# Performance work log

Hardware: AMD Instinct MI355X
Metric: run time of the kernel (lower is better)

The kernel has to match this reference:

```python
import jax, jax.numpy as jnp
import numpy as np

H = 1024      # hidden_size
NH = 16       # num_heads
HD = H // NH  # head_dim


def setup_inputs() -> dict:
    key = jax.random.key(0)
    ks = jax.random.split(key, 12)
    inp = {
        "query": jax.random.normal(ks[0], (4, 1024, H), dtype=jnp.float32),
        "key": jax.random.normal(ks[1], (4, 2048, H), dtype=jnp.float32),
        "value": jax.random.normal(ks[2], (4, 2048, H), dtype=jnp.float32),
        "key_padding_mask": jax.random.randint(ks[3], (4, 2048), 0, 2, dtype=jnp.int32),
        # learned parameters (torch Linear: y = x @ W.T + b); we store W already transposed
        "Wq": jax.random.normal(ks[4], (H, H), dtype=jnp.float32) * (1.0 / np.sqrt(H)),
        "bq": jnp.zeros((H,), dtype=jnp.float32),
        "Wk": jax.random.normal(ks[5], (H, H), dtype=jnp.float32) * (1.0 / np.sqrt(H)),
        "bk": jnp.zeros((H,), dtype=jnp.float32),
        "Wv": jax.random.normal(ks[6], (H, H), dtype=jnp.float32) * (1.0 / np.sqrt(H)),
        "bv": jnp.zeros((H,), dtype=jnp.float32),
        "Wo": jax.random.normal(ks[7], (H, H), dtype=jnp.float32) * (1.0 / np.sqrt(H)),
        "bo": jnp.zeros((H,), dtype=jnp.float32),
    }
    return inp


def reference(query, key, value, key_padding_mask, Wq, bq, Wk, bk, Wv, bv, Wo, bo):
    B, Sq, _ = query.shape
    Sk = key.shape[1]
    scaling = HD ** -0.5
    # projections -> [B, NH, S, HD]
    q = (query @ Wq + bq).reshape(B, Sq, NH, HD).transpose(0, 2, 1, 3)
    k = (key @ Wk + bk).reshape(B, Sk, NH, HD).transpose(0, 2, 1, 3)
    v = (value @ Wv + bv).reshape(B, Sk, NH, HD).transpose(0, 2, 1, 3)
    # scores [B, NH, Sq, Sk]
    scores = jnp.einsum("bhqd,bhkd->bhqk", q, k) * scaling
    # mask: positions where key_padding_mask == 0 are ignored
    scores = jnp.where((key_padding_mask == 0)[:, None, None, :], -jnp.inf, scores)
    attn = jax.nn.softmax(scores, axis=-1)
    # dropout is identity in eval mode
    out = jnp.einsum("bhqk,bhkd->bhqd", attn, v)
    out = out.transpose(0, 2, 1, 3).reshape(B, Sq, H)
    return out @ Wo + bo
```

## Files before the change

kernel.cpp:

```cpp
#include <hip/hip_runtime.h>
#include <hip/hip_fp16.h>
#include <math.h>

#define B_ 4
#define SQ 1024
#define SK 2048
#define HH 1024
#define NHEAD 16
#define HDIM 64

typedef _Float16 f16;
typedef __attribute__((ext_vector_type(8))) _Float16 f16x8;
typedef __attribute__((ext_vector_type(4))) _Float16 f16x4;
typedef __attribute__((ext_vector_type(4))) float f32x4;
typedef unsigned int u32;

#define GLOAD_LDS16(gp, lp) __builtin_amdgcn_global_load_lds( \
    (const __attribute__((address_space(1))) u32*)(gp),        \
    (__attribute__((address_space(3))) u32*)(lp), 16, 0, 0)
#define GLOAD_LDS4(gp, lp) __builtin_amdgcn_global_load_lds(  \
    (const __attribute__((address_space(1))) u32*)(gp),        \
    (__attribute__((address_space(3))) u32*)(lp), 4, 0, 0)

__global__ __launch_bounds__(256) void prep_k(
    const float* __restrict__ q, const float* __restrict__ k,
    const float* __restrict__ v,
    const float* __restrict__ W0, const float* __restrict__ W1,
    const float* __restrict__ W2, const float* __restrict__ W3,
    const int* __restrict__ mask,
    f16* __restrict__ qo, f16* __restrict__ ko, f16* __restrict__ vo,
    f16* __restrict__ WT, float* __restrict__ pbias)
{
    __shared__ f16 t[64 * 80];
    const int bid = blockIdx.x, tid = threadIdx.x;
    if (bid < 10240) {
        int i = bid * 256 + tid;
        const float* src; f16* dst; int j;
        if (i < 524288)       { src = q; dst = qo; j = i; }
        else if (i < 1572864) { src = k; dst = ko; j = i - 524288; }
        else                  { src = v; dst = vo; j = i - 1572864; }
        float4 a = ((const float4*)src)[(size_t)j * 2];
        float4 b = ((const float4*)src)[(size_t)j * 2 + 1];
        f16x8 o;
        o[0] = (f16)a.x; o[1] = (f16)a.y; o[2] = (f16)a.z; o[3] = (f16)a.w;
        o[4] = (f16)b.x; o[5] = (f16)b.y; o[6] = (f16)b.z; o[7] = (f16)b.w;
        *(f16x8*)(dst + (size_t)j * 8) = o;
    } else if (bid < 11264) {
        int id = bid - 10240;
        int z = id >> 8, idx = id & 255;
        const float* W = z == 0 ? W0 : z == 1 ? W1 : z == 2 ? W2 : W3;
        f16* out = WT + (size_t)z * HH * HH;
        const int r0 = (idx >> 4) * 64, c0 = (idx & 15) * 64;
#pragma unroll
        for (int p = 0; p < 4; p++) {
            int s = p * 256 + tid;
            int row = s >> 4, u = s & 15;
            float4 a = *(const float4*)(W + (size_t)(r0 + row) * HH + c0 + u * 4);
            f16x4 vv;
            vv[0] = (f16)a.x; vv[1] = (f16)a.y; vv[2] = (f16)a.z; vv[3] = (f16)a.w;
            *(f16x4*)(t + row * 80 + u * 4) = vv;
        }
        __syncthreads();
#pragma unroll
        for (int p = 0; p < 2; p++) {
            int s = p * 256 + tid;
            int n = s >> 3, u = s & 7;
            f16x8 vv;
#pragma unroll
            for (int j = 0; j < 8; j++) vv[j] = t[(u * 8 + j) * 80 + n];
            *(f16x8*)(out + (size_t)(c0 + n) * HH + r0 + u * 8) = vv;
        }
    } else {
        int j = (bid - 11264) * 256 + tid;
        pbias[j] = mask[j] ? 0.f : -1e30f;
    }
}

template <int TM, int OUTMODE>
__device__ __forceinline__ void gemm_body(
    const f16* __restrict__ A, const f16* __restrict__ BT,
    const float* __restrict__ bias, void* __restrict__ Cout,
    int bid, int nwg, f16* sA, f16* sB)
{
    const int tid = threadIdx.x, lane = tid & 63, w = tid >> 6;
    const int swz = (bid & 7) * (nwg >> 3) + (bid >> 3);
    const int m0 = (swz >> 3) * TM;
    const int n0 = (swz & 7) * 128;
    const int wr = w >> 1, wc = w & 1;
    const int ql = lane & 15, g = lane >> 4;
    const int N = 1024, K = 1024;
    const int MF = TM / 32;
    const int ABUF = TM * 32;
    f32x4 acc[MF][4] = {};

    auto stageA = [&](int buf, int k0) {
#pragma unroll
        for (int p = 0; p < TM / 64; p++) {
            int s = p * 256 + tid;
            int row = s >> 2, us = ((s & 3) ^ ((row >> 1) & 3)) * 8;
            GLOAD_LDS16(A + (size_t)(m0 + row) * K + k0 + us,
                        sA + buf * ABUF + (p * 256 + w * 64) * 8);
        }
    };
    auto stageB = [&](int buf, int k0) {
#pragma unroll
        for (int p = 0; p < 2; p++) {
            int s = p * 256 + tid;
            int row = s >> 2, us = ((s & 3) ^ ((row >> 1) & 3)) * 8;
            GLOAD_LDS16(BT + (size_t)(n0 + row) * K + k0 + us,
                        sB + buf * 4096 + (p * 256 + w * 64) * 8);
        }
    };
    auto compute = [&](int buf) {
        f16x8 af[MF], bf[4];
#pragma unroll
        for (int m = 0; m < MF; m++) {
            int row = wr * (TM / 2) + m * 16 + ql;
            af[m] = *(const f16x8*)(sA + buf * ABUF + row * 32 + ((g ^ ((row >> 1) & 3)) * 8));
        }
#pragma unroll
        for (int n = 0; n < 4; n++) {
            int row = wc * 64 + n * 16 + ql;
            bf[n] = *(const f16x8*)(sB + buf * 4096 + row * 32 + ((g ^ ((row >> 1) & 3)) * 8));
        }
#pragma unroll
        for (int m = 0; m < MF; m++)
#pragma unroll
            for (int n = 0; n < 4; n++)
                acc[m][n] = __builtin_amdgcn_mfma_f32_16x16x32_f16(af[m], bf[n], acc[m][n], 0, 0, 0);
    };

    stageA(0, 0);
    stageB(0, 0);
    int cur = 0;
#pragma unroll 1
    for (int k0 = 0; k0 < K; k0 += 32) {
        __syncthreads();
        if (k0 + 32 < K) { stageA(cur ^ 1, k0 + 32); stageB(cur ^ 1, k0 + 32); }
        compute(cur);
        cur ^= 1;
    }

    float bv[4];
#pragma unroll
    for (int n = 0; n < 4; n++) bv[n] = bias[n0 + wc * 64 + n * 16 + ql];
#pragma unroll
    for (int m = 0; m < MF; m++) {
        int row0 = m0 + wr * (TM / 2) + m * 16 + g * 4;
#pragma unroll
        for (int n = 0; n < 4; n++) {
            int col = n0 + wc * 64 + n * 16 + ql;
            if (OUTMODE == 2) {
                int bb = row0 >> 11, kk = row0 & 2047;
                int hh = col >> 6, dd = col & 63;
                f16x4 vv;
#pragma unroll
                for (int e = 0; e < 4; e++) vv[e] = (f16)(acc[m][n][e] + bv[n]);
                *(f16x4*)((f16*)Cout + ((size_t)(bb * NHEAD + hh) * HDIM + dd) * SK + kk) = vv;
            } else if (OUTMODE == 1) {
#pragma unroll
                for (int e = 0; e < 4; e++)
                    ((f16*)Cout)[(size_t)(row0 + e) * N + col] = (f16)(acc[m][n][e] + bv[n]);
            } else {
#pragma unroll
                for (int e = 0; e < 4; e++)
                    ((float*)Cout)[(size_t)(row0 + e) * N + col] = acc[m][n][e] + bv[n];
            }
        }
    }
}

__global__ __launch_bounds__(256) void qkv_gemm_k(
    const f16* __restrict__ qc, const f16* __restrict__ kc,
    const f16* __restrict__ vc, const f16* __restrict__ wT,
    const float* __restrict__ bq, const float* __restrict__ bk,
    const float* __restrict__ bv,
    f16* __restrict__ qp, f16* __restrict__ kp, f16* __restrict__ vt)
{
    __shared__ f16 sA[2 * 4096];
    __shared__ f16 sB[2 * 4096];
    const int bid = blockIdx.x;
    const size_t M1 = 1024 * 1024;
    if (bid < 512)
        gemm_body<64, 1>(qc, wT, bq, qp, bid, 512, sA, sB);
    else if (bid < 1024)
        gemm_body<128, 1>(kc, wT + M1, bk, kp, bid - 512, 512, sA, sB);
    else
        gemm_body<128, 2>(vc, wT + 2 * M1, bv, vt, bid - 1024, 512, sA, sB);
}

__global__ __launch_bounds__(256) void o_gemm_k(
    const f16* __restrict__ ctx, const f16* __restrict__ wT,
    const float* __restrict__ bo, float* __restrict__ out)
{
    __shared__ f16 sA[2 * 4096];
    __shared__ f16 sB[2 * 4096];
    gemm_body<64, 0>(ctx, wT, bo, out, blockIdx.x, 512, sA, sB);
}

#define SC2 0.18033688f
#define THR2 11.5f

__global__ __launch_bounds__(512, 4) void attn_mfma_k(
    const f16* __restrict__ qp,
    const f16* __restrict__ kp,
    const f16* __restrict__ vt,
    const float* __restrict__ pbias,
    f16* __restrict__ ctx)
{
    const int flat = ((int)blockIdx.x & 7) * 64 + ((int)blockIdx.x >> 3);
    const int qt = flat & 7, h = (flat >> 3) & 15, b = flat >> 7;
    const int q0 = qt * 128;
    const int tid = threadIdx.x, lane = tid & 63, w = tid >> 6;
    const int ql = lane & 15, g = lane >> 4;

    __shared__ f16 ks[2 * 4096];
    __shared__ f16 vs[2 * 4096];
    __shared__ f16 plds[8][16 * 64];
    __shared__ float sbias[2][64];

    const f16* kbase = kp + (size_t)b * SK * HH + h * HDIM;
    const f16* vbase = vt + ((size_t)(b * NHEAD + h)) * HDIM * SK;
    const float* bbase = pbias + b * SK;

    f16x8 qf[2];
    {
        const f16* qb = qp + ((size_t)(b * SQ + q0 + w * 16 + ql)) * HH + h * HDIM + g * 8;
        qf[0] = *(const f16x8*)qb;
        qf[1] = *(const f16x8*)(qb + 32);
    }

    auto stageKV = [&](int buf, int kt) {
        int r = tid >> 3, ulg = ((tid & 7) ^ (r & 7)) * 8;
        GLOAD_LDS16(kbase + (size_t)(kt + r) * HH + ulg, ks + buf * 4096 + w * 512);
        GLOAD_LDS16(vbase + (size_t)r * SK + kt + ulg,   vs + buf * 4096 + w * 512);
        if (w == 0) GLOAD_LDS4(bbase + kt + lane, &sbias[buf][0]);
    };

    f32x4 oacc[4] = {};
    float mrun = -1e30f, lrun = 0.f;
    f16* pw = &plds[w][0];

    auto tile = [&](const f16* kb, const f16* vb, const float* sb,
                    bool pf_en, int pbuf, int pkt) {
        __syncthreads();
        if (pf_en) stageKV(pbuf, pkt);

        f32x4 sacc[4] = {};
        __builtin_amdgcn_s_setprio(1);
#pragma unroll
        for (int n = 0; n < 4; n++) {
            int key = n * 16 + ql;
#pragma unroll
            for (int df = 0; df < 2; df++) {
                int u = df * 4 + g;
                f16x8 kf = *(const f16x8*)(kb + key * 64 + ((u ^ (key & 7)) * 8));
                sacc[n] = __builtin_amdgcn_mfma_f32_16x16x32_f16(kf, qf[df], sacc[n], 0, 0, 0);
            }
        }
        __builtin_amdgcn_s_setprio(0);

        float sv[4][4];
        float mt = -1e30f;
#pragma unroll
        for (int n = 0; n < 4; n++) {
            float4 b4 = *(const float4*)&sb[n * 16 + g * 4];
            float barr[4] = {b4.x, b4.y, b4.z, b4.w};
#pragma unroll
            for (int e = 0; e < 4; e++) {
                float s = fmaf(sacc[n][e], SC2, barr[e]);
                sv[n][e] = s;
                mt = fmaxf(mt, s);
            }
        }
        mt = fmaxf(mt, __shfl_xor(mt, 16, 64));
        mt = fmaxf(mt, __shfl_xor(mt, 32, 64));

        if (__any(mt > mrun + THR2)) {
            float mnew = fmaxf(mrun, mt);
            float alpha = __builtin_amdgcn_exp2f(mrun - mnew);
            mrun = mnew;
            lrun *= alpha;
            float al[4];
#pragma unroll
            for (int e = 0; e < 4; e++) al[e] = __shfl(alpha, g * 4 + e, 64);
#pragma unroll
            for (int df = 0; df < 4; df++)
#pragma unroll
                for (int e = 0; e < 4; e++) oacc[df][e] *= al[e];
        }

        float tsum = 0.f;
#pragma unroll
        for (int n = 0; n < 4; n++) {
            float p0 = __builtin_amdgcn_exp2f(sv[n][0] - mrun);
            float p1 = __builtin_amdgcn_exp2f(sv[n][1] - mrun);
            float p2 = __builtin_amdgcn_exp2f(sv[n][2] - mrun);
            float p3 = __builtin_amdgcn_exp2f(sv[n][3] - mrun);
            tsum += (p0 + p1) + (p2 + p3);
            f16x4 pv4;
            pv4[0] = (f16)p0; pv4[1] = (f16)p1; pv4[2] = (f16)p2; pv4[3] = (f16)p3;
            *(f16x4*)(pw + ql * 64 + (((2 * n + (g >> 1)) ^ (ql & 7)) * 8) + (g & 1) * 4) = pv4;
        }
        tsum += __shfl_xor(tsum, 16, 64);
        tsum += __shfl_xor(tsum, 32, 64);
        lrun += tsum;

        __builtin_amdgcn_s_setprio(1);
#pragma unroll
        for (int t = 0; t < 2; t++) {
            f16x8 pf = *(const f16x8*)(pw + ql * 64 + (((t * 4 + g) ^ (ql & 7)) * 8));
#pragma unroll
            for (int df = 0; df < 4; df++) {
                int d = df * 16 + ql;
                int u = t * 4 + g;
                f16x8 vf = *(const f16x8*)(vb + d * 64 + ((u ^ (d & 7)) * 8));
                oacc[df] = __builtin_amdgcn_mfma_f32_16x16x32_f16(pf, vf, oacc[df], 0, 0, 0);
            }
        }
        __builtin_amdgcn_s_setprio(0);
    };

    stageKV(0, 0);
#pragma unroll 1
    for (int kt = 0; kt < SK; kt += 128) {
        tile(ks, vs, sbias[0], true, 1, kt + 64);
        tile(ks + 4096, vs + 4096, sbias[1], kt + 128 < SK, 0, kt + 128);
    }

    float linv[4];
#pragma unroll
    for (int e = 0; e < 4; e++) {
        float lv = __shfl(lrun, g * 4 + e, 64);
        linv[e] = 1.f / lv;
    }
    f16* ob = ctx + ((size_t)(b * SQ + q0 + w * 16)) * HH + h * HDIM;
#pragma unroll
    for (int df = 0; df < 4; df++)
#pragma unroll
        for (int e = 0; e < 4; e++)
            ob[(size_t)(g * 4 + e) * HH + df * 16 + ql] = (f16)(oacc[df][e] * linv[e]);
}

extern "C" void kernel_launch(void* const* d_in, const int* in_sizes, int n_in,
                              void* d_out, int out_size, void* d_ws, size_t ws_size,
                              hipStream_t stream) {
    const float* query = (const float*)d_in[0];
    const float* key   = (const float*)d_in[1];
    const float* value = (const float*)d_in[2];
    const int*   mask  = (const int*)d_in[3];
    const float* Wq = (const float*)d_in[4];
    const float* bq = (const float*)d_in[5];
    const float* Wk = (const float*)d_in[6];
    const float* bk = (const float*)d_in[7];
    const float* Wv = (const float*)d_in[8];
    const float* bv = (const float*)d_in[9];
    const float* Wo = (const float*)d_in[10];
    const float* bo = (const float*)d_in[11];
    float* out = (float*)d_out;

    const size_t M1 = 1024 * 1024;
    f16* qcast = (f16*)d_ws;
    f16* kcast = qcast + 4 * M1;
    f16* vcast = kcast + 8 * M1;
    f16* wT    = vcast + 8 * M1;
    f16* qp    = wT + 4 * M1;
    f16* kp    = qp + 4 * M1;
    f16* vt    = kp + 8 * M1;
    float* pbias = (float*)(vt + 8 * M1);
    f16* ctx   = qcast;

    dim3 blk(256);

    prep_k<<<dim3(11296), blk, 0, stream>>>(query, key, value, Wq, Wk, Wv, Wo,
                                            mask, qcast, kcast, vcast, wT, pbias);

    qkv_gemm_k<<<dim3(1536), blk, 0, stream>>>(qcast, kcast, vcast, wT,
                                               bq, bk, bv, qp, kp, vt);

    attn_mfma_k<<<dim3(512), dim3(512), 0, stream>>>(qp, kp, vt, pbias, ctx);

    o_gemm_k<<<dim3(512), blk, 0, stream>>>(ctx, wT + 3 * M1, bo, out);
}
```

Baseline: 166.4 us.

## Pipeline QKV GEMM loads two stages ahead with explicit waitcnt barriers

Adds a PIPE variant of the GEMM body that prefetches two k-steps ahead. It uses explicit vmcnt/lgkmcnt waits and raw s_barrier with sched barriers in place of __syncthreads, so global-to-LDS loads overlap with MFMA compute. The Q projection also moves from a 64-row tile to a 128-row tile, which cuts the QKV grid from 1536 to 1280 blocks. The vmcnt(4) count assumes a fixed number of loads per stage, and it risks a race if that assumption does not hold. The output GEMM keeps the old schedule.

```diff
diff --git a/kernel.cpp b/kernel.cpp
--- a/kernel.cpp
+++ b/kernel.cpp
@@ -21,6 +21,11 @@
 #define GLOAD_LDS4(gp, lp) __builtin_amdgcn_global_load_lds(  \
     (const __attribute__((address_space(1))) u32*)(gp),        \
     (__attribute__((address_space(3))) u32*)(lp), 4, 0, 0)
+
+#define VMWAIT(N) asm volatile("s_waitcnt vmcnt(" #N ")" ::: "memory")
+#define LGKM0     asm volatile("s_waitcnt lgkmcnt(0)" ::: "memory")
+#define SCHB      __builtin_amdgcn_sched_barrier(0)
+#define BAR()     __builtin_amdgcn_s_barrier()
 
 __global__ __launch_bounds__(256) void prep_k(
     const float* __restrict__ q, const float* __restrict__ k,
@@ -76,7 +81,7 @@
     }
 }
 
-template <int TM, int OUTMODE>
+template <int TM, int OUTMODE, int PIPE>
 __device__ __forceinline__ void gemm_body(
     const f16* __restrict__ A, const f16* __restrict__ BT,
     const float* __restrict__ bias, void* __restrict__ Cout,
@@ -130,15 +135,36 @@
                 acc[m][n] = __builtin_amdgcn_mfma_f32_16x16x32_f16(af[m], bf[n], acc[m][n], 0, 0, 0);
     };
 
-    stageA(0, 0);
-    stageB(0, 0);
-    int cur = 0;
+    if (PIPE) {
+        stageA(0, 0);  stageB(0, 0);
+        stageA(1, 32); stageB(1, 32);
+        VMWAIT(4); SCHB; BAR(); SCHB;
+        int cur = 0;
 #pragma unroll 1
-    for (int k0 = 0; k0 < K; k0 += 32) {
-        __syncthreads();
-        if (k0 + 32 < K) { stageA(cur ^ 1, k0 + 32); stageB(cur ^ 1, k0 + 32); }
-        compute(cur);
-        cur ^= 1;
+        for (int k0 = 0; k0 < K; k0 += 32) {
+            compute(cur);
+            LGKM0; SCHB; BAR(); SCHB;
+            if (k0 + 64 < K) {
+                stageA(cur, k0 + 64);
+                stageB(cur, k0 + 64);
+                VMWAIT(4);
+            } else {
+                VMWAIT(0);
+            }
+            SCHB; BAR(); SCHB;
+            cur ^= 1;
+        }
+    } else {
+        stageA(0, 0);
+        stageB(0, 0);
+        int cur = 0;
+#pragma unroll 1
+        for (int k0 = 0; k0 < K; k0 += 32) {
+            __syncthreads();
+            if (k0 + 32 < K) { stageA(cur ^ 1, k0 + 32); stageB(cur ^ 1, k0 + 32); }
+            compute(cur);
+            cur ^= 1;
+        }
     }
 
     float bv[4];
@@ -181,12 +207,12 @@
     __shared__ f16 sB[2 * 4096];
     const int bid = blockIdx.x;
     const size_t M1 = 1024 * 1024;
-    if (bid < 512)
-        gemm_body<64, 1>(qc, wT, bq, qp, bid, 512, sA, sB);
-    else if (bid < 1024)
-        gemm_body<128, 1>(kc, wT + M1, bk, kp, bid - 512, 512, sA, sB);
+    if (bid < 256)
+        gemm_body<128, 1, 1>(qc, wT, bq, qp, bid, 256, sA, sB);
+    else if (bid < 768)
+        gemm_body<128, 1, 1>(kc, wT + M1, bk, kp, bid - 256, 512, sA, sB);
     else
-        gemm_body<128, 2>(vc, wT + 2 * M1, bv, vt, bid - 1024, 512, sA, sB);
+        gemm_body<128, 2, 1>(vc, wT + 2 * M1, bv, vt, bid - 768, 512, sA, sB);
 }
 
 __global__ __launch_bounds__(256) void o_gemm_k(
@@ -195,7 +221,7 @@
 {
     __shared__ f16 sA[2 * 4096];
     __shared__ f16 sB[2 * 4096];
-    gemm_body<64, 0>(ctx, wT, bo, out, blockIdx.x, 512, sA, sB);
+    gemm_body<64, 0, 0>(ctx, wT, bo, out, blockIdx.x, 512, sA, sB);
 }
 
 #define SC2 0.18033688f
@@ -375,7 +401,7 @@
     prep_k<<<dim3(11296), blk, 0, stream>>>(query, key, value, Wq, Wk, Wv, Wo,
                                             mask, qcast, kcast, vcast, wT, pbias);
 
-    qkv_gemm_k<<<dim3(1536), blk, 0, stream>>>(qcast, kcast, vcast, wT,
+    qkv_gemm_k<<<dim3(1280), blk, 0, stream>>>(qcast, kcast, vcast, wT,
                                                bq, bk, bv, qp, kp, vt);
 
     attn_mfma_k<<<dim3(512), dim3(512), 0, stream>>>(qp, kp, vt, pbias, ctx);
```

Result: slower. 170.4 us (+2.4%).

## Load QKV GEMM operands directly into registers, dropping LDS staging

Applied to the files above, without the earlier changes.

The QKV projection GEMM no longer stages tiles through shared memory with double buffering. Each wave now loads its A and B fragments straight from global memory into registers and feeds them to MFMA. The Q projection moves to 128-row tiles, cutting its workgroup count. The goal is to remove LDS traffic and barriers, at the cost of redundant global/L2 reads across waves and uncoalesced 16-byte row loads. The output GEMM keeps LDS staging, specialised to 64-row tiles.

```diff
diff --git a/kernel.cpp b/kernel.cpp
--- a/kernel.cpp
+++ b/kernel.cpp
@@ -76,31 +76,107 @@
     }
 }
 
-template <int TM, int OUTMODE>
-__device__ __forceinline__ void gemm_body(
+template <int OUTMODE>
+__device__ __forceinline__ void gemm_reg(
     const f16* __restrict__ A, const f16* __restrict__ BT,
     const float* __restrict__ bias, void* __restrict__ Cout,
-    int bid, int nwg, f16* sA, f16* sB)
+    int bid, int nwg)
 {
-    const int tid = threadIdx.x, lane = tid & 63, w = tid >> 6;
+    const int lane = threadIdx.x & 63, w = threadIdx.x >> 6;
     const int swz = (bid & 7) * (nwg >> 3) + (bid >> 3);
-    const int m0 = (swz >> 3) * TM;
+    const int m0 = (swz >> 3) * 128;
     const int n0 = (swz & 7) * 128;
     const int wr = w >> 1, wc = w & 1;
     const int ql = lane & 15, g = lane >> 4;
     const int N = 1024, K = 1024;
-    const int MF = TM / 32;
-    const int ABUF = TM * 32;
-    f32x4 acc[MF][4] = {};
+    f32x4 acc[4][4] = {};
+
+    const f16* Ab = A + (size_t)(m0 + wr * 64 + ql) * K + g * 8;
+    const f16* Bb = BT + (size_t)(n0 + wc * 64 + ql) * K + g * 8;
+
+#pragma unroll 2
+    for (int k0 = 0; k0 < K; k0 += 32) {
+        f16x8 af[4], bf[4];
+#pragma unroll
+        for (int m = 0; m < 4; m++)
+            af[m] = *(const f16x8*)(Ab + (size_t)(m * 16) * K + k0);
+#pragma unroll
+        for (int n = 0; n < 4; n++)
+            bf[n] = *(const f16x8*)(Bb + (size_t)(n * 16) * K + k0);
+#pragma unroll
+        for (int m = 0; m < 4; m++)
+#pragma unroll
+            for (int n = 0; n < 4; n++)
+                acc[m][n] = __builtin_amdgcn_mfma_f32_16x16x32_f16(af[m], bf[n], acc[m][n], 0, 0, 0);
+    }
+
+    float bv[4];
+#pragma unroll
+    for (int n = 0; n < 4; n++) bv[n] = bias[n0 + wc * 64 + n * 16 + ql];
+#pragma unroll
+    for (int m = 0; m < 4; m++) {
+        int row0 = m0 + wr * 64 + m * 16 + g * 4;
+#pragma unroll
+        for (int n = 0; n < 4; n++) {
+            int col = n0 + wc * 64 + n * 16 + ql;
+            if (OUTMODE == 2) {
+                int bb = row0 >> 11, kk = row0 & 2047;
+                int hh = col >> 6, dd = col & 63;
+                f16x4 vv;
+#pragma unroll
+                for (int e = 0; e < 4; e++) vv[e] = (f16)(acc[m][n][e] + bv[n]);
+                *(f16x4*)((f16*)Cout + ((size_t)(bb * NHEAD + hh) * HDIM + dd) * SK + kk) = vv;
+            } else if (OUTMODE == 1) {
+#pragma unroll
+                for (int e = 0; e < 4; e++)
+                    ((f16*)Cout)[(size_t)(row0 + e) * N + col] = (f16)(acc[m][n][e] + bv[n]);
+            } else {
+#pragma unroll
+                for (int e = 0; e < 4; e++)
+                    ((float*)Cout)[(size_t)(row0 + e) * N + col] = acc[m][n][e] + bv[n];
+            }
+        }
+    }
+}
+
+__global__ __launch_bounds__(256) void qkv_gemm_k(
+    const f16* __restrict__ qc, const f16* __restrict__ kc,
+    const f16* __restrict__ vc, const f16* __restrict__ wT,
+    const float* __restrict__ bq, const float* __restrict__ bk,
+    const float* __restrict__ bv,
+    f16* __restrict__ qp, f16* __restrict__ kp, f16* __restrict__ vt)
+{
+    const int bid = blockIdx.x;
+    const size_t M1 = 1024 * 1024;
+    if (bid < 256)
+        gemm_reg<1>(qc, wT, bq, qp, bid, 256);
+    else if (bid < 768)
+        gemm_reg<1>(kc, wT + M1, bk, kp, bid - 256, 512);
+    else
+        gemm_reg<2>(vc, wT + 2 * M1, bv, vt, bid - 768, 512);
+}
+
+__global__ __launch_bounds__(256) void o_gemm_k(
+    const f16* __restrict__ A, const f16* __restrict__ BT,
+    const float* __restrict__ bias, float* __restrict__ out)
+{
+    __shared__ f16 sA[2 * 2048];
+    __shared__ f16 sB[2 * 4096];
+    const int tid = threadIdx.x, lane = tid & 63, w = tid >> 6;
+    const int bid = blockIdx.x, nwg = 512;
+    const int swz = (bid & 7) * (nwg >> 3) + (bid >> 3);
+    const int m0 = (swz >> 3) * 64;
+    const int n0 = (swz & 7) * 128;
+    const int wr = w >> 1, wc = w & 1;
+    const int ql = lane & 15, g = lane >> 4;
+    const int N = 1024, K = 1024;
+    f32x4 acc[2][4] = {};
 
     auto stageA = [&](int buf, int k0) {
-#pragma unroll
-        for (int p = 0; p < TM / 64; p++) {
-            int s = p * 256 + tid;
-            int row = s >> 2, us = ((s & 3) ^ ((row >> 1) & 3)) * 8;
-            GLOAD_LDS16(A + (size_t)(m0 + row) * K + k0 + us,
-                        sA + buf * ABUF + (p * 256 + w * 64) * 8);
-        }
+        int s = tid;
+        int row = s >> 2, us = ((s & 3) ^ ((row >> 1) & 3)) * 8;
+        GLOAD_LDS16(A + (size_t)(m0 + row) * K + k0 + us,
+                    sA + buf * 2048 + (w * 64) * 8);
     };
     auto stageB = [&](int buf, int k0) {
 #pragma unroll
@@ -112,11 +188,11 @@
         }
     };
     auto compute = [&](int buf) {
-        f16x8 af[MF], bf[4];
-#pragma unroll
-        for (int m = 0; m < MF; m++) {
-            int row = wr * (TM / 2) + m * 16 + ql;
-            af[m] = *(const f16x8*)(sA + buf * ABUF + row * 32 + ((g ^ ((row >> 1) & 3)) * 8));
+        f16x8 af[2], bf[4];
+#pragma unroll
+        for (int m = 0; m < 2; m++) {
+            int row = wr * 32 + m * 16 + ql;
+            af[m] = *(const f16x8*)(sA + buf * 2048 + row * 32 + ((g ^ ((row >> 1) & 3)) * 8));
         }
 #pragma unroll
         for (int n = 0; n < 4; n++) {
@@ -124,7 +200,7 @@
             bf[n] = *(const f16x8*)(sB + buf * 4096 + row * 32 + ((g ^ ((row >> 1) & 3)) * 8));
         }
 #pragma unroll
-        for (int m = 0; m < MF; m++)
+        for (int m = 0; m < 2; m++)
 #pragma unroll
             for (int n = 0; n < 4; n++)
                 acc[m][n] = __builtin_amdgcn_mfma_f32_16x16x32_f16(af[m], bf[n], acc[m][n], 0, 0, 0);
@@ -145,57 +221,16 @@
 #pragma unroll
     for (int n = 0; n < 4; n++) bv[n] = bias[n0 + wc * 64 + n * 16 + ql];
 #pragma unroll
-    for (int m = 0; m < MF; m++) {
-        int row0 = m0 + wr * (TM / 2) + m * 16 + g * 4;
+    for (int m = 0; m < 2; m++) {
+        int row0 = m0 + wr * 32 + m * 16 + g * 4;
 #pragma unroll
         for (int n = 0; n < 4; n++) {
             int col = n0 + wc * 64 + n * 16 + ql;
-            if (OUTMODE == 2) {
-                int bb = row0 >> 11, kk = row0 & 2047;
-                int hh = col >> 6, dd = col & 63;
-                f16x4 vv;
-#pragma unroll
-                for (int e = 0; e < 4; e++) vv[e] = (f16)(acc[m][n][e] + bv[n]);
-                *(f16x4*)((f16*)Cout + ((size_t)(bb * NHEAD + hh) * HDIM + dd) * SK + kk) = vv;
-            } else if (OUTMODE == 1) {
-#pragma unroll
-                for (int e = 0; e < 4; e++)
-                    ((f16*)Cout)[(size_t)(row0 + e) * N + col] = (f16)(acc[m][n][e] + bv[n]);
-            } else {
-#pragma unroll
-                for (int e = 0; e < 4; e++)
-                    ((float*)Cout)[(size_t)(row0 + e) * N + col] = acc[m][n][e] + bv[n];
-            }
-        }
-    }
-}
-
-__global__ __launch_bounds__(256) void qkv_gemm_k(
-    const f16* __restrict__ qc, const f16* __restrict__ kc,
-    const f16* __restrict__ vc, const f16* __restrict__ wT,
-    const float* __restrict__ bq, const float* __restrict__ bk,
-    const float* __restrict__ bv,
-    f16* __restrict__ qp, f16* __restrict__ kp, f16* __restrict__ vt)
-{
-    __shared__ f16 sA[2 * 4096];
-    __shared__ f16 sB[2 * 4096];
-    const int bid = blockIdx.x;
-    const size_t M1 = 1024 * 1024;
-    if (bid < 512)
-        gemm_body<64, 1>(qc, wT, bq, qp, bid, 512, sA, sB);
-    else if (bid < 1024)
-        gemm_body<128, 1>(kc, wT + M1, bk, kp, bid - 512, 512, sA, sB);
-    else
-        gemm_body<128, 2>(vc, wT + 2 * M1, bv, vt, bid - 1024, 512, sA, sB);
-}
-
-__global__ __launch_bounds__(256) void o_gemm_k(
-    const f16* __restrict__ ctx, const f16* __restrict__ wT,
-    const float* __restrict__ bo, float* __restrict__ out)
-{
-    __shared__ f16 sA[2 * 4096];
-    __shared__ f16 sB[2 * 4096];
-    gemm_body<64, 0>(ctx, wT, bo, out, blockIdx.x, 512, sA, sB);
+#pragma unroll
+            for (int e = 0; e < 4; e++)
+                out[(size_t)(row0 + e) * N + col] = acc[m][n][e] + bv[n];
+        }
+    }
 }
 
 #define SC2 0.18033688f
@@ -375,7 +410,7 @@
     prep_k<<<dim3(11296), blk, 0, stream>>>(query, key, value, Wq, Wk, Wv, Wo,
                                             mask, qcast, kcast, vcast, wT, pbias);
 
-    qkv_gemm_k<<<dim3(1536), blk, 0, stream>>>(qcast, kcast, vcast, wT,
+    qkv_gemm_k<<<dim3(1280), blk, 0, stream>>>(qcast, kcast, vcast, wT,
                                                bq, bk, bv, qp, kp, vt);
 
     attn_mfma_k<<<dim3(512), dim3(512), 0, stream>>>(qp, kp, vt, pbias, ctx);
```

Result: slower. 256.1 us (+53.9%).
